# Kernel optimization log

Measured on AMD Instinct MI355X. Metric: run time of the kernel, lower is better.

## Reference

```python
import jax, jax.numpy as jnp
import numpy as np

N = 50000      # current-level nodes
N_NEXT = 2000  # next-level nodes
E = 1600000    # directed edges (before self-loops)
D_IN = 128
D_OUT = 128
LN_EPS = 1e-5


def setup_inputs() -> dict:
    key = jax.random.key(0)
    ks = jax.random.split(key, 12)
    curr_h = jax.random.normal(ks[0], (N, D_IN), dtype=jnp.float32)
    next_h = jax.random.normal(ks[1], (N_NEXT, D_IN), dtype=jnp.float32)
    inc = jax.random.uniform(ks[2], (N, N_NEXT), dtype=jnp.float32)
    src = jax.random.randint(ks[3], (E,), 0, N, dtype=jnp.int64)
    dst = jax.random.randint(ks[4], (E,), 0, N, dtype=jnp.int64)
    s = 1.0 / np.sqrt(D_IN)
    W_conv = jax.random.normal(ks[5], (D_IN, D_OUT), dtype=jnp.float32) * s
    b_conv = jnp.zeros((D_OUT,), dtype=jnp.float32)
    W_fus = jax.random.normal(ks[6], (D_IN, D_OUT), dtype=jnp.float32) * s
    b_fus = jnp.zeros((D_OUT,), dtype=jnp.float32)
    conv_w = jax.random.uniform(ks[7], (D_OUT,), dtype=jnp.float32)
    topDown_w = jax.random.uniform(ks[8], (D_OUT,), dtype=jnp.float32)
    ln_gamma = jnp.ones((D_OUT,), dtype=jnp.float32)
    ln_beta = jnp.zeros((D_OUT,), dtype=jnp.float32)
    return {
        "curr_h": curr_h, "next_h": next_h, "inc": inc,
        "src": src, "dst": dst,
        "W_conv": W_conv, "b_conv": b_conv,
        "W_fus": W_fus, "b_fus": b_fus,
        "conv_w": conv_w, "topDown_w": topDown_w,
        "ln_gamma": ln_gamma, "ln_beta": ln_beta,
    }


def _graph_conv(x, W, b, src_sl, dst_sl, norm_out, norm_in):
    # DGL GraphConv, norm='both': D_out^{-1/2} on src, sum-aggregate, D_in^{-1/2} on dst.
    h = x @ W                               # [N, D_OUT]
    h = h * norm_out[:, None]
    agg = jax.ops.segment_sum(h[src_sl], dst_sl, num_segments=N)  # SpMM
    return agg * norm_in[:, None] + b


def reference(curr_h, next_h, inc, src, dst,
              W_conv, b_conv, W_fus, b_fus,
              conv_w, topDown_w, ln_gamma, ln_beta):
    # dgl.add_self_loop
    loop = jnp.arange(N, dtype=src.dtype)
    src_sl = jnp.concatenate([src, loop])
    dst_sl = jnp.concatenate([dst, loop])
    ones = jnp.ones_like(src_sl, dtype=jnp.float32)
    out_deg = jax.ops.segment_sum(ones, src_sl, num_segments=N)
    in_deg = jax.ops.segment_sum(ones, dst_sl, num_segments=N)
    norm_out = jax.lax.rsqrt(out_deg)  # >=1 due to self-loops
    norm_in = jax.lax.rsqrt(in_deg)

    conv_layer = _graph_conv(curr_h, W_conv, b_conv, src_sl, dst_sl, norm_out, norm_in) * conv_w[None, :]
    fused_in = inc @ next_h  # dense incidence matmul [N, D_IN]
    top_down = _graph_conv(fused_in, W_fus, b_fus, src_sl, dst_sl, norm_out, norm_in) * topDown_w[None, :]

    result = conv_layer + top_down
    # LayerNorm over last dim
    mu = jnp.mean(result, axis=-1, keepdims=True)
    var = jnp.mean((result - mu) ** 2, axis=-1, keepdims=True)
    result = (result - mu) * jax.lax.rsqrt(var + LN_EPS) * ln_gamma + ln_beta
    # dropout p=0.0 (eval) -> identity; activation ReLU
    return jax.nn.relu(result)
```

## Files before the change

kernel.cpp:

```cpp
#include <hip/hip_runtime.h>
#include <hip/hip_bf16.h>

#define N_NODES   50000
#define EDGES     1600000
#define D         128
#define K_INC     2000
#define K_TOT     2128
#define K_PAD     2176
#define LN_EPS    1e-5f

typedef float f32x4 __attribute__((ext_vector_type(4)));
typedef short short8 __attribute__((ext_vector_type(8)));

__device__ __forceinline__ ushort f2bf(float x) {
    return __hip_bfloat16_raw(__float2bfloat16(x)).x;
}
__device__ __forceinline__ float bf_lo(uint v) { return __uint_as_float(v << 16); }
__device__ __forceinline__ float bf_hi(uint v) { return __uint_as_float(v & 0xffff0000u); }

__global__ void probe_kernel(const int* __restrict__ src, int* __restrict__ flag) {
    __shared__ int any_nonzero;
    if (threadIdx.x == 0) any_nonzero = 0;
    __syncthreads();
    int v = src[threadIdx.x * 2 + 1];
    if (v != 0) any_nonzero = 1;
    __syncthreads();
    if (threadIdx.x == 0) flag[0] = any_nonzero ? 0 : 1;
}

__global__ void zero_kernel(int* __restrict__ p, int n) {
    int i = blockIdx.x * 256 + threadIdx.x;
    if (i < n) p[i] = 0;
}

__global__ void deg_kernel(const int* __restrict__ src, const int* __restrict__ dst,
                           const int* __restrict__ flag,
                           int* __restrict__ out_deg, int* __restrict__ in_cnt) {
    int e = blockIdx.x * 256 + threadIdx.x;
    int st = 1 + flag[0];
    if (e < EDGES) {
        atomicAdd(&out_deg[src[e * st]], 1);
        atomicAdd(&in_cnt[dst[e * st]], 1);
    }
}

__global__ __launch_bounds__(1024) void scan_kernel(const int* __restrict__ cnt,
                                                    int* __restrict__ row_start) {
    __shared__ int buf[1024];
    int t = threadIdx.x;
    const int N = N_NODES;
    int chunk = (N + 1023) / 1024;
    int lo = t * chunk, hi = min(lo + chunk, N);
    int s = 0;
    for (int i = lo; i < hi; ++i) s += cnt[i];
    buf[t] = s;
    __syncthreads();
    for (int off = 1; off < 1024; off <<= 1) {
        int v = (t >= off) ? buf[t - off] : 0;
        __syncthreads();
        buf[t] += v;
        __syncthreads();
    }
    int run = (t > 0) ? buf[t - 1] : 0;
    for (int i = lo; i < hi; ++i) { row_start[i] = run; run += cnt[i]; }
    if (t == 1023) row_start[N] = buf[1023];
}

__global__ void fill_kernel(const int* __restrict__ src, const int* __restrict__ dst,
                            const int* __restrict__ flag,
                            const int* __restrict__ row_start, int* __restrict__ cursor,
                            int* __restrict__ csr_src) {
    int e = blockIdx.x * 256 + threadIdx.x;
    int st = 1 + flag[0];
    if (e < EDGES) {
        int d = dst[e * st];
        int pos = atomicAdd(&cursor[d], 1);
        csr_src[row_start[d] + pos] = src[e * st];
    }
}

__global__ __launch_bounds__(128) void p_kernel(
    const float* __restrict__ next_h, const float* __restrict__ W_fus,
    const float* __restrict__ topDown_w, const float* __restrict__ W_conv,
    const float* __restrict__ conv_w, ushort* __restrict__ PbT) {
    int k = blockIdx.x, n = threadIdx.x;
    float v;
    if (k < K_INC) {
        __shared__ float nh[D];
        nh[n] = next_h[k * D + n];
        __syncthreads();
        float acc = 0.f;
        for (int j = 0; j < D; ++j) acc += nh[j] * W_fus[j * D + n];
        v = acc * topDown_w[n];
    } else if (k < K_TOT) {
        v = W_conv[(k - K_INC) * D + n] * conv_w[n];
    } else {
        v = 0.f;
    }
    PbT[(size_t)n * K_PAD + k] = f2bf(v);
}

__global__ __launch_bounds__(256) void gemm_kernel(
    const float* __restrict__ inc, const float* __restrict__ curr_h,
    const ushort* __restrict__ PbT, const int* __restrict__ out_deg,
    ushort* __restrict__ Zs) {
    __shared__ ushort As[64][72];
    __shared__ ushort Bs[128][72];
    const int N = N_NODES;
    int tid = threadIdx.x;
    int wave = tid >> 6, lane = tid & 63;
    int wm = wave >> 1, wn = wave & 1;
    int r = lane & 15, q = lane >> 4;
    int rowBase = blockIdx.x * 64;

    f32x4 acc[2][4] = {};

    for (int kt = 0; kt < K_PAD / 64; ++kt) {
        int k0 = kt * 64;
        __syncthreads();
#pragma unroll
        for (int it = 0; it < 4; ++it) {
            int id = tid + it * 256;
            int arow = id >> 4, c4 = id & 15;
            int gk = k0 + c4 * 4;
            int grow = rowBase + arow; if (grow >= N) grow = N - 1;
            float4 va;
            if (gk < K_INC)      va = *(const float4*)(inc + (size_t)grow * K_INC + gk);
            else if (gk < K_TOT) va = *(const float4*)(curr_h + (size_t)grow * D + (gk - K_INC));
            else                 va = make_float4(0.f, 0.f, 0.f, 0.f);
            ushort4 hb;
            hb.x = f2bf(va.x); hb.y = f2bf(va.y); hb.z = f2bf(va.z); hb.w = f2bf(va.w);
            *(ushort4*)&As[arow][c4 * 4] = hb;
        }
#pragma unroll
        for (int it = 0; it < 4; ++it) {
            int id = tid + it * 256;
            int brow = id >> 3, c8 = id & 7;
            uint4 vb = *(const uint4*)(PbT + (size_t)brow * K_PAD + k0 + c8 * 8);
            *(uint4*)&Bs[brow][c8 * 8] = vb;
        }
        __syncthreads();
#pragma unroll
        for (int kk = 0; kk < 2; ++kk) {
            short8 af[2], bfr[4];
#pragma unroll
            for (int mi = 0; mi < 2; ++mi)
                af[mi] = *(const short8*)&As[wm * 32 + mi * 16 + r][kk * 32 + q * 8];
#pragma unroll
            for (int ni = 0; ni < 4; ++ni)
                bfr[ni] = *(const short8*)&Bs[wn * 64 + ni * 16 + r][kk * 32 + q * 8];
#pragma unroll
            for (int mi = 0; mi < 2; ++mi)
#pragma unroll
                for (int ni = 0; ni < 4; ++ni)
                    acc[mi][ni] = __builtin_amdgcn_mfma_f32_16x16x32_bf16(af[mi], bfr[ni], acc[mi][ni], 0, 0, 0);
        }
    }

#pragma unroll
    for (int mi = 0; mi < 2; ++mi) {
#pragma unroll
        for (int j = 0; j < 4; ++j) {
            int grow = rowBase + wm * 32 + mi * 16 + q * 4 + j;
            if (grow < N) {
                float no = rsqrtf((float)(out_deg[grow] + 1));
#pragma unroll
                for (int ni = 0; ni < 4; ++ni) {
                    int col = wn * 64 + ni * 16 + r;
                    Zs[(size_t)grow * D + col] = f2bf(acc[mi][ni][j] * no);
                }
            }
        }
    }
}

__global__ __launch_bounds__(256) void agg_ln_kernel(
    const ushort* __restrict__ Zs, const int* __restrict__ row_start,
    const int* __restrict__ csr_src,
    const float* __restrict__ b_conv, const float* __restrict__ b_fus,
    const float* __restrict__ conv_w, const float* __restrict__ topDown_w,
    const float* __restrict__ gamma, const float* __restrict__ beta,
    float* __restrict__ out) {
    int wid = threadIdx.x >> 6, lane = threadIdx.x & 63;
    int node = blockIdx.x * 4 + wid;
    if (node >= N_NODES) return;
    int c0 = lane * 2;

    uint v = *(const uint*)(Zs + (size_t)node * D + c0);
    float a0 = bf_lo(v), a1 = bf_hi(v);
    int beg = row_start[node], end = row_start[node + 1];
    int e = beg;
    for (; e + 1 < end; e += 2) {
        int s0 = csr_src[e], s1 = csr_src[e + 1];
        uint v0 = *(const uint*)(Zs + (size_t)s0 * D + c0);
        uint v1 = *(const uint*)(Zs + (size_t)s1 * D + c0);
        a0 += bf_lo(v0) + bf_lo(v1);
        a1 += bf_hi(v0) + bf_hi(v1);
    }
    if (e < end) {
        int s0 = csr_src[e];
        uint v0 = *(const uint*)(Zs + (size_t)s0 * D + c0);
        a0 += bf_lo(v0); a1 += bf_hi(v0);
    }
    float nin = rsqrtf((float)(end - beg + 1));
    float y0 = a0 * nin + b_conv[c0] * conv_w[c0] + b_fus[c0] * topDown_w[c0];
    float y1 = a1 * nin + b_conv[c0 + 1] * conv_w[c0 + 1] + b_fus[c0 + 1] * topDown_w[c0 + 1];

    float s1v = y0 + y1, s2v = y0 * y0 + y1 * y1;
#pragma unroll
    for (int off = 1; off < 64; off <<= 1) {
        s1v += __shfl_xor(s1v, off);
        s2v += __shfl_xor(s2v, off);
    }
    float mu = s1v * (1.f / D);
    float var = s2v * (1.f / D) - mu * mu;
    float rstd = rsqrtf(var + LN_EPS);
    float r0 = (y0 - mu) * rstd * gamma[c0] + beta[c0];
    float r1 = (y1 - mu) * rstd * gamma[c0 + 1] + beta[c0 + 1];
    *(float2*)(out + (size_t)node * D + c0) = make_float2(fmaxf(r0, 0.f), fmaxf(r1, 0.f));
}

extern "C" void kernel_launch(void* const* d_in, const int* in_sizes, int n_in,
                              void* d_out, int out_size, void* d_ws, size_t ws_size,
                              hipStream_t stream) {
    const float* curr_h    = (const float*)d_in[0];
    const float* next_h    = (const float*)d_in[1];
    const float* inc       = (const float*)d_in[2];
    const int*   src       = (const int*)d_in[3];
    const int*   dst       = (const int*)d_in[4];
    const float* W_conv    = (const float*)d_in[5];
    const float* b_conv    = (const float*)d_in[6];
    const float* W_fus     = (const float*)d_in[7];
    const float* b_fus     = (const float*)d_in[8];
    const float* conv_w    = (const float*)d_in[9];
    const float* topDown_w = (const float*)d_in[10];
    const float* ln_gamma  = (const float*)d_in[11];
    const float* ln_beta   = (const float*)d_in[12];

    const int N = N_NODES;
    const int E = EDGES;

    char* p = (char*)d_ws;
    ushort* Zs = (ushort*)p;     p += (size_t)N * D * sizeof(ushort);
    ushort* PbT = (ushort*)p;    p += (size_t)D * K_PAD * 2;
    int* out_deg   = (int*)p;    p += (size_t)N * 4;
    int* in_cnt    = (int*)p;    p += (size_t)N * 4;
    int* cursor    = (int*)p;    p += (size_t)N * 4;
    int* row_start = (int*)p;    p += (size_t)(N + 1) * 4;
    int* idx_flag  = (int*)p;    p += 256;
    int* csr_src   = (int*)p;    p += (size_t)E * 4;

    probe_kernel<<<1, 1024, 0, stream>>>(src, idx_flag);
    zero_kernel<<<(3 * N + 255) / 256, 256, 0, stream>>>(out_deg, 3 * N);
    deg_kernel<<<(E + 255) / 256, 256, 0, stream>>>(src, dst, idx_flag, out_deg, in_cnt);
    scan_kernel<<<1, 1024, 0, stream>>>(in_cnt, row_start);
    fill_kernel<<<(E + 255) / 256, 256, 0, stream>>>(src, dst, idx_flag, row_start, cursor, csr_src);
    p_kernel<<<K_PAD, 128, 0, stream>>>(next_h, W_fus, topDown_w, W_conv, conv_w, PbT);
    gemm_kernel<<<(N + 63) / 64, 256, 0, stream>>>(inc, curr_h, PbT, out_deg, Zs);
    agg_ln_kernel<<<(N + 3) / 4, 256, 0, stream>>>(Zs, row_start, csr_src,
                                                   b_conv, b_fus, conv_w, topDown_w,
                                                   ln_gamma, ln_beta, (float*)d_out);
}
```

Measured before the change: 0.9997 ms.

## Double-buffer GEMM with direct-to-LDS B loads, batch p_kernel, shuffle CSR indices

The GEMM now double-buffers its A and B tiles. The next A tile is prefetched into registers and the B tile is loaded straight into LDS with global_load_lds under an XOR swizzle, so loads overlap the MFMA work and the extra barrier goes away. p_kernel computes 16 k-rows per block instead of one. The aggregation kernel loads 64 CSR indices per wave at a time and broadcasts them with shuffles, with four gathers in flight. Together these aim to hide memory latency in the GEMM, which streams the large incidence matrix, and in the gather, at the cost of more LDS and register pressure.

```diff
diff --git a/kernel.cpp b/kernel.cpp
--- a/kernel.cpp
+++ b/kernel.cpp
@@ -7,16 +7,22 @@
 #define K_INC     2000
 #define K_TOT     2128
 #define K_PAD     2176
+#define KTILES    34
 #define LN_EPS    1e-5f
 
 typedef float f32x4 __attribute__((ext_vector_type(4)));
 typedef short short8 __attribute__((ext_vector_type(8)));
+typedef ushort ushort8v __attribute__((ext_vector_type(8)));
 
 __device__ __forceinline__ ushort f2bf(float x) {
     return __hip_bfloat16_raw(__float2bfloat16(x)).x;
 }
 __device__ __forceinline__ float bf_lo(uint v) { return __uint_as_float(v << 16); }
 __device__ __forceinline__ float bf_hi(uint v) { return __uint_as_float(v & 0xffff0000u); }
+
+#define GLOAD_LDS16(gp, lp) \
+    __builtin_amdgcn_global_load_lds((const __attribute__((address_space(1))) void*)(gp), \
+                                     (__attribute__((address_space(3))) void*)(lp), 16, 0, 0)
 
 __global__ void probe_kernel(const int* __restrict__ src, int* __restrict__ flag) {
     __shared__ int any_nonzero;
@@ -79,33 +85,45 @@
     }
 }
 
+#define PKB 16
 __global__ __launch_bounds__(128) void p_kernel(
     const float* __restrict__ next_h, const float* __restrict__ W_fus,
     const float* __restrict__ topDown_w, const float* __restrict__ W_conv,
     const float* __restrict__ conv_w, ushort* __restrict__ PbT) {
-    int k = blockIdx.x, n = threadIdx.x;
-    float v;
-    if (k < K_INC) {
-        __shared__ float nh[D];
-        nh[n] = next_h[k * D + n];
-        __syncthreads();
-        float acc = 0.f;
-        for (int j = 0; j < D; ++j) acc += nh[j] * W_fus[j * D + n];
-        v = acc * topDown_w[n];
-    } else if (k < K_TOT) {
-        v = W_conv[(k - K_INC) * D + n] * conv_w[n];
+    int n = threadIdx.x;
+    int k0 = blockIdx.x * PKB;
+    if (k0 < K_INC) {
+        float acc[PKB];
+#pragma unroll
+        for (int t = 0; t < PKB; ++t) acc[t] = 0.f;
+        for (int j = 0; j < D; ++j) {
+            float w = W_fus[(size_t)j * D + n];
+#pragma unroll
+            for (int t = 0; t < PKB; ++t)
+                acc[t] += next_h[(size_t)(k0 + t) * D + j] * w;
+        }
+        float tw = topDown_w[n];
+#pragma unroll
+        for (int t = 0; t < PKB; ++t)
+            PbT[(size_t)n * K_PAD + k0 + t] = f2bf(acc[t] * tw);
+    } else if (k0 < K_TOT) {
+        float cw = conv_w[n];
+#pragma unroll
+        for (int t = 0; t < PKB; ++t)
+            PbT[(size_t)n * K_PAD + k0 + t] = f2bf(W_conv[(size_t)(k0 + t - K_INC) * D + n] * cw);
     } else {
-        v = 0.f;
-    }
-    PbT[(size_t)n * K_PAD + k] = f2bf(v);
-}
-
-__global__ __launch_bounds__(256) void gemm_kernel(
+#pragma unroll
+        for (int t = 0; t < PKB; ++t)
+            PbT[(size_t)n * K_PAD + k0 + t] = 0;
+    }
+}
+
+__global__ __launch_bounds__(256, 3) void gemm_kernel(
     const float* __restrict__ inc, const float* __restrict__ curr_h,
     const ushort* __restrict__ PbT, const int* __restrict__ out_deg,
     ushort* __restrict__ Zs) {
-    __shared__ ushort As[64][72];
-    __shared__ ushort Bs[128][72];
+    __shared__ __align__(16) ushort As[2][64][72];
+    __shared__ __align__(16) ushort Bs[2][128 * 64];
     const int N = N_NODES;
     int tid = threadIdx.x;
     int wave = tid >> 6, lane = tid & 63;
@@ -114,47 +132,80 @@
     int rowBase = blockIdx.x * 64;
 
     f32x4 acc[2][4] = {};
-
-    for (int kt = 0; kt < K_PAD / 64; ++kt) {
+    float4 aReg[2][2];
+
+    auto stage_issue = [&](int kt, int nb) {
         int k0 = kt * 64;
-        __syncthreads();
+#pragma unroll
+        for (int it = 0; it < 2; ++it) {
+            int u = tid + it * 256;
+            int arow = u >> 3, c8 = u & 7;
+            int gk = k0 + c8 * 8;
+            int grow = rowBase + arow; if (grow >= N) grow = N - 1;
+            if (gk < K_INC) {
+                const float4* p4 = (const float4*)(inc + (size_t)grow * K_INC + gk);
+                aReg[it][0] = p4[0]; aReg[it][1] = p4[1];
+            } else if (gk < K_TOT) {
+                const float4* p4 = (const float4*)(curr_h + (size_t)grow * D + (gk - K_INC));
+                aReg[it][0] = p4[0]; aReg[it][1] = p4[1];
+            } else {
+                aReg[it][0] = make_float4(0.f, 0.f, 0.f, 0.f);
+                aReg[it][1] = make_float4(0.f, 0.f, 0.f, 0.f);
+            }
+        }
 #pragma unroll
         for (int it = 0; it < 4; ++it) {
-            int id = tid + it * 256;
-            int arow = id >> 4, c4 = id & 15;
-            int gk = k0 + c4 * 4;
-            int grow = rowBase + arow; if (grow >= N) grow = N - 1;
-            float4 va;
-            if (gk < K_INC)      va = *(const float4*)(inc + (size_t)grow * K_INC + gk);
-            else if (gk < K_TOT) va = *(const float4*)(curr_h + (size_t)grow * D + (gk - K_INC));
-            else                 va = make_float4(0.f, 0.f, 0.f, 0.f);
-            ushort4 hb;
-            hb.x = f2bf(va.x); hb.y = f2bf(va.y); hb.z = f2bf(va.z); hb.w = f2bf(va.w);
-            *(ushort4*)&As[arow][c4 * 4] = hb;
-        }
-#pragma unroll
-        for (int it = 0; it < 4; ++it) {
-            int id = tid + it * 256;
-            int brow = id >> 3, c8 = id & 7;
-            uint4 vb = *(const uint4*)(PbT + (size_t)brow * K_PAD + k0 + c8 * 8);
-            *(uint4*)&Bs[brow][c8 * 8] = vb;
-        }
-        __syncthreads();
+            int chunk = tid + it * 256;
+            int n = chunk >> 3;
+            int c16 = (chunk & 7) << 4;
+            int gb = c16 ^ ((n & 7) << 4);
+            const char* gp = (const char*)PbT + (size_t)n * (K_PAD * 2) + (size_t)(k0 * 2) + gb;
+            char* lp = (char*)(&Bs[nb][0]) + it * 4096 + wave * 1024;
+            GLOAD_LDS16(gp, lp);
+        }
+    };
+    auto stage_write = [&](int nb) {
+#pragma unroll
+        for (int it = 0; it < 2; ++it) {
+            int u = tid + it * 256;
+            int arow = u >> 3, c8 = u & 7;
+            const float* f = (const float*)&aReg[it][0];
+            ushort8v hv;
+#pragma unroll
+            for (int j = 0; j < 8; ++j) hv[j] = f2bf(f[j]);
+            *(ushort8v*)&As[nb][arow][c8 * 8] = hv;
+        }
+    };
+
+    stage_issue(0, 0);
+    stage_write(0);
+    __syncthreads();
+
+    int cur = 0;
+    for (int kt = 0; kt < KTILES; ++kt) {
+        int nb = cur ^ 1;
+        if (kt + 1 < KTILES) stage_issue(kt + 1, nb);
 #pragma unroll
         for (int kk = 0; kk < 2; ++kk) {
             short8 af[2], bfr[4];
 #pragma unroll
             for (int mi = 0; mi < 2; ++mi)
-                af[mi] = *(const short8*)&As[wm * 32 + mi * 16 + r][kk * 32 + q * 8];
-#pragma unroll
-            for (int ni = 0; ni < 4; ++ni)
-                bfr[ni] = *(const short8*)&Bs[wn * 64 + ni * 16 + r][kk * 32 + q * 8];
+                af[mi] = *(const short8*)&As[cur][wm * 32 + mi * 16 + r][kk * 32 + q * 8];
+#pragma unroll
+            for (int ni = 0; ni < 4; ++ni) {
+                int brow = wn * 64 + ni * 16 + r;
+                int bcol = (kk * 64 + q * 16) ^ ((r & 7) << 4);
+                bfr[ni] = *(const short8*)((const char*)&Bs[cur][0] + brow * 128 + bcol);
+            }
 #pragma unroll
             for (int mi = 0; mi < 2; ++mi)
 #pragma unroll
                 for (int ni = 0; ni < 4; ++ni)
                     acc[mi][ni] = __builtin_amdgcn_mfma_f32_16x16x32_bf16(af[mi], bfr[ni], acc[mi][ni], 0, 0, 0);
         }
+        if (kt + 1 < KTILES) stage_write(nb);
+        __syncthreads();
+        cur = nb;
     }
 
 #pragma unroll
@@ -189,19 +240,30 @@
     uint v = *(const uint*)(Zs + (size_t)node * D + c0);
     float a0 = bf_lo(v), a1 = bf_hi(v);
     int beg = row_start[node], end = row_start[node + 1];
-    int e = beg;
-    for (; e + 1 < end; e += 2) {
-        int s0 = csr_src[e], s1 = csr_src[e + 1];
-        uint v0 = *(const uint*)(Zs + (size_t)s0 * D + c0);
-        uint v1 = *(const uint*)(Zs + (size_t)s1 * D + c0);
-        a0 += bf_lo(v0) + bf_lo(v1);
-        a1 += bf_hi(v0) + bf_hi(v1);
-    }
-    if (e < end) {
-        int s0 = csr_src[e];
-        uint v0 = *(const uint*)(Zs + (size_t)s0 * D + c0);
-        a0 += bf_lo(v0); a1 += bf_hi(v0);
-    }
+
+    for (int base = beg; base < end; base += 64) {
+        int rem = end - base;
+        int cnt = rem < 64 ? rem : 64;
+        int idx = 0;
+        if (base + lane < end) idx = csr_src[base + lane];
+        int i = 0;
+        for (; i + 4 <= cnt; i += 4) {
+            int s0 = __shfl(idx, i),     s1 = __shfl(idx, i + 1);
+            int s2 = __shfl(idx, i + 2), s3 = __shfl(idx, i + 3);
+            uint v0 = *(const uint*)(Zs + (size_t)s0 * D + c0);
+            uint v1 = *(const uint*)(Zs + (size_t)s1 * D + c0);
+            uint v2 = *(const uint*)(Zs + (size_t)s2 * D + c0);
+            uint v3 = *(const uint*)(Zs + (size_t)s3 * D + c0);
+            a0 += bf_lo(v0) + bf_lo(v1) + bf_lo(v2) + bf_lo(v3);
+            a1 += bf_hi(v0) + bf_hi(v1) + bf_hi(v2) + bf_hi(v3);
+        }
+        for (; i < cnt; ++i) {
+            int s0 = __shfl(idx, i);
+            uint v0 = *(const uint*)(Zs + (size_t)s0 * D + c0);
+            a0 += bf_lo(v0); a1 += bf_hi(v0);
+        }
+    }
+
     float nin = rsqrtf((float)(end - beg + 1));
     float y0 = a0 * nin + b_conv[c0] * conv_w[c0] + b_fus[c0] * topDown_w[c0];
     float y1 = a1 * nin + b_conv[c0 + 1] * conv_w[c0 + 1] + b_fus[c0 + 1] * topDown_w[c0 + 1];
@@ -255,7 +317,7 @@
     deg_kernel<<<(E + 255) / 256, 256, 0, stream>>>(src, dst, idx_flag, out_deg, in_cnt);
     scan_kernel<<<1, 1024, 0, stream>>>(in_cnt, row_start);
     fill_kernel<<<(E + 255) / 256, 256, 0, stream>>>(src, dst, idx_flag, row_start, cursor, csr_src);
-    p_kernel<<<K_PAD, 128, 0, stream>>>(next_h, W_fus, topDown_w, W_conv, conv_w, PbT);
+    p_kernel<<<K_PAD / PKB, 128, 0, stream>>>(next_h, W_fus, topDown_w, W_conv, conv_w, PbT);
     gemm_kernel<<<(N + 63) / 64, 256, 0, stream>>>(inc, curr_h, PbT, out_deg, Zs);
     agg_ln_kernel<<<(N + 3) / 4, 256, 0, stream>>>(Zs, row_start, csr_src,
                                                    b_conv, b_fus, conv_w, topDown_w,
```

Result: faster. 954.0 us (-4.6%).
